# Performance work log

Hardware: AMD Instinct MI355X
Metric: run time of the kernel (lower is better)

Reference implementation:

```python
import jax, jax.numpy as jnp
import numpy as np

B, P, M, N, H = 2, 2048, 1024, 16, 64
NEG = 1e10


def setup_inputs() -> dict:
    key = jax.random.key(0)
    ks = jax.random.split(key, 8)
    std = 0.02
    return {
        "x": jax.random.normal(ks[0], (B, P, M), jnp.float32),
        "kernel_query": std * jax.random.normal(ks[1], (N, M, H), jnp.float32),
        "bias_query": jnp.zeros((N, H), jnp.float32),
        "kernel_key": std * jax.random.normal(ks[2], (N, M, H), jnp.float32),
        "bias_key": jnp.zeros((N, H), jnp.float32),
        "kernel_value": std * jax.random.normal(ks[3], (N, M, H), jnp.float32),
        "bias_value": jnp.zeros((N, H), jnp.float32),
        "kernel_out": std * jax.random.normal(ks[4], (N, H, M), jnp.float32),
        "bias_out": jnp.zeros((M,), jnp.float32),
    }


def reference(x, kernel_query, bias_query, kernel_key, bias_key,
              kernel_value, bias_value, kernel_out, bias_out):
    # per-head projections: [b,p,m] x [n,m,h] -> [b,p,n,h]
    q = jnp.einsum('bpm,nmh->bpnh', x, kernel_query) + bias_query
    k = jnp.einsum('bpm,nmh->bpnh', x, kernel_key) + bias_key
    v = jnp.einsum('bpm,nmh->bpnh', x, kernel_value) + bias_value

    # explicit score matrix [b,n,pq,pk]
    scores = jnp.einsum('bqnh,bknh->bnqk', q, k) / jnp.sqrt(jnp.float32(H))
    # faithful reproduction of original (inverted) mask: keep strictly-upper
    # triangle, subtract 1e10 elsewhere
    p = scores.shape[-1]
    mask = jnp.triu(jnp.ones((p, p), scores.dtype), k=1)  # [pq,pk]
    masked = scores * mask - NEG * (1.0 - mask)
    attn = jax.nn.softmax(masked, axis=-1)

    z = jnp.einsum('bknh,bnqk->bqnh', v, attn)
    return jnp.einsum('bqnh,nhm->bqm', z, kernel_out) + bias_out
```

## Files before the change

kernel.cpp:

```cpp
#include <hip/hip_runtime.h>

typedef __attribute__((ext_vector_type(8))) __bf16 bf16x8;
typedef __attribute__((ext_vector_type(4))) float  f32x4;
typedef unsigned short u16;
typedef unsigned int   u32;

__device__ __forceinline__ u16 f2b(float f) {
  u32 u = __builtin_bit_cast(u32, f);
  u32 r = (u + 0x7FFFu + ((u >> 16) & 1u)) >> 16;
  return (u16)r;
}

typedef __attribute__((address_space(3))) void lds_void;
typedef const __attribute__((address_space(1))) void gbl_void;

__device__ __forceinline__ void gload_lds16(const u16* g, u16* l) {
  __builtin_amdgcn_global_load_lds((gbl_void*)g, (lds_void*)l, 16, 0, 0);
}

#define QSCALE 0.18033688011112042f
#define MFIX   4.328085122666891f

__global__ __launch_bounds__(256) void prep_x(const float* __restrict__ x,
                                              u16* __restrict__ xb) {
  int i = blockIdx.x * 256 + threadIdx.x;
  float4 v = ((const float4*)x)[i];
  ushort4 o;
  o.x = f2b(v.x); o.y = f2b(v.y); o.z = f2b(v.z); o.w = f2b(v.w);
  ((ushort4*)xb)[i] = o;
}

__global__ __launch_bounds__(256) void tcast(const float* __restrict__ src,
                                             u16* __restrict__ dst,
                                             int R, int C, int sstride, int dstride,
                                             int smat, int dmat) {
  __shared__ float t[64][65];
  src += (size_t)blockIdx.y * smat;
  dst += (size_t)blockIdx.y * dmat;
  int ntr = R >> 6;
  int rt = blockIdx.x % ntr, ct = blockIdx.x / ntr;
  int r0 = rt * 64, c0 = ct * 64;
  int tid = threadIdx.x;
  int rr = tid >> 2, q = tid & 3;
#pragma unroll
  for (int i = 0; i < 4; ++i) {
    float4 v = *(const float4*)&src[(size_t)(r0 + rr) * sstride + c0 + q * 16 + i * 4];
    t[rr][q * 16 + i * 4 + 0] = v.x;
    t[rr][q * 16 + i * 4 + 1] = v.y;
    t[rr][q * 16 + i * 4 + 2] = v.z;
    t[rr][q * 16 + i * 4 + 3] = v.w;
  }
  __syncthreads();
  int cc = rr;
#pragma unroll
  for (int i = 0; i < 4; ++i) {
    ushort4 o;
    o.x = f2b(t[q * 16 + i * 4 + 0][cc]);
    o.y = f2b(t[q * 16 + i * 4 + 1][cc]);
    o.z = f2b(t[q * 16 + i * 4 + 2][cc]);
    o.w = f2b(t[q * 16 + i * 4 + 3][cc]);
    *(ushort4*)&dst[(size_t)(c0 + cc) * dstride + r0 + q * 16 + i * 4] = o;
  }
}

template <int KDIM>
__device__ __forceinline__ void gemm_main(const u16* __restrict__ A,
                                          const u16* __restrict__ Bm,
                                          int R0, int C0,
                                          u16* As, u16* Bs, f32x4 (&acc)[4][4]) {
  int tid = threadIdx.x;
  int w = tid >> 6, l = tid & 63;
  int lr = l & 15, lg = l >> 4;
  int wr = w >> 1, wc = w & 1;
  for (int k0 = 0; k0 < KDIM; k0 += 32) {
#pragma unroll
    for (int i = 0; i < 2; ++i) {
      int t = w * 2 + i;
      gload_lds16(A  + (size_t)(R0 + t * 16 + (l >> 2)) * KDIM + k0 + (l & 3) * 8, &As[t * 512]);
      gload_lds16(Bm + (size_t)(C0 + t * 16 + (l >> 2)) * KDIM + k0 + (l & 3) * 8, &Bs[t * 512]);
    }
    __syncthreads();
    bf16x8 af[4], bfr[4];
#pragma unroll
    for (int mi = 0; mi < 4; ++mi)
      af[mi] = *(const bf16x8*)&As[(wr * 64 + mi * 16 + lr) * 32 + lg * 8];
#pragma unroll
    for (int ni = 0; ni < 4; ++ni)
      bfr[ni] = *(const bf16x8*)&Bs[(wc * 64 + ni * 16 + lr) * 32 + lg * 8];
#pragma unroll
    for (int mi = 0; mi < 4; ++mi)
#pragma unroll
      for (int ni = 0; ni < 4; ++ni)
        acc[mi][ni] = __builtin_amdgcn_mfma_f32_16x16x32_bf16(af[mi], bfr[ni], acc[mi][ni], 0, 0, 0);
    __syncthreads();
  }
}

__global__ __launch_bounds__(256) void gemm_qkv(const u16* __restrict__ xb,
                                                const u16* __restrict__ wbt,
                                                const float* __restrict__ bq,
                                                const float* __restrict__ bk,
                                                const float* __restrict__ bv,
                                                u16* __restrict__ qb,
                                                u16* __restrict__ kbf,
                                                u16* __restrict__ vtb) {
  __shared__ __align__(16) u16 As[128 * 32];
  __shared__ __align__(16) u16 Bs[128 * 32];
  f32x4 acc[4][4];
#pragma unroll
  for (int mi = 0; mi < 4; ++mi)
#pragma unroll
    for (int ni = 0; ni < 4; ++ni) acc[mi][ni] = (f32x4){0.f, 0.f, 0.f, 0.f};

  int bid = blockIdx.x;
  int rt = bid & 31, ct = bid >> 5;
  int R0 = rt * 128, C0 = ct * 128;
  gemm_main<1024>(xb, wbt, R0, C0, As, Bs, acc);

  int tid = threadIdx.x;
  int w = tid >> 6, l = tid & 63;
  int lr = l & 15, lg = l >> 4;
  int wr = w >> 1, wc = w & 1;
#pragma unroll
  for (int ni = 0; ni < 4; ++ni) {
    int col = C0 + wc * 64 + ni * 16 + lr;
    int proj = col >> 10;
    int within = col & 1023;
    int n = within >> 6, h = within & 63;
    const float* bias = (proj == 0) ? bq : (proj == 1 ? bk : bv);
    float badd = bias[within];
    float scl = (proj == 0) ? QSCALE : 1.0f;
#pragma unroll
    for (int mi = 0; mi < 4; ++mi) {
#pragma unroll
      for (int r = 0; r < 4; ++r) {
        int row = R0 + wr * 64 + mi * 16 + lg * 4 + r;
        int b = row >> 11, p = row & 2047;
        int bn = b * 16 + n;
        u16 u = f2b((acc[mi][ni][r] + badd) * scl);
        if (proj == 0)      qb [((size_t)bn * 2048 + p) * 64 + h] = u;
        else if (proj == 1) kbf[((size_t)bn * 2048 + p) * 64 + h] = u;
        else                vtb[(((size_t)bn * 32 + (p >> 6)) * 64 + h) * 64 + (p & 63)] = u;
      }
    }
  }
}

__global__ __launch_bounds__(256) void mean_v(const u16* __restrict__ vtb,
                                              u16* __restrict__ zb) {
  __shared__ float red[4][64];
  int bn = blockIdx.x;
  int w = threadIdx.x >> 6, h = threadIdx.x & 63;
  const u16* base = vtb + (size_t)bn * 131072 + (size_t)h * 64;
  float acc = 0.f;
  for (int pb = w; pb < 32; pb += 4) {
    const u16* r = base + (size_t)pb * 4096;
#pragma unroll
    for (int c = 0; c < 8; ++c) {
      bf16x8 v = *(const bf16x8*)(r + c * 8);
#pragma unroll
      for (int j = 0; j < 8; ++j) acc += (float)v[j];
    }
  }
  red[w][h] = acc;
  __syncthreads();
  if (w == 0) {
    float s = (red[0][h] + red[1][h] + red[2][h] + red[3][h]) * (1.0f / 2048.0f);
    int b = bn >> 4, n = bn & 15;
    zb[((size_t)(b * 2048 + 2047) * 16 + n) * 64 + h] = f2b(s);
  }
}

#define ATTN_STEP(BUFC, MASKED)                                                \
  {                                                                            \
    if (t + 1 < trips) {                                                       \
      gload_lds16(sk,       &Ks[BUFC ^ 1][w * 1024]);                          \
      gload_lds16(sk + 512, &Ks[BUFC ^ 1][w * 1024 + 512]);                    \
      gload_lds16(sv,       &Vs[BUFC ^ 1][w * 1024]);                          \
      gload_lds16(sv + 512, &Vs[BUFC ^ 1][w * 1024 + 512]);                    \
      sk += 4096; sv += 4096;                                                  \
      asm volatile("s_waitcnt vmcnt(4)" ::: "memory");                         \
    } else {                                                                   \
      asm volatile("s_waitcnt vmcnt(0)" ::: "memory");                         \
    }                                                                          \
    __builtin_amdgcn_s_barrier();                                              \
    asm volatile("" ::: "memory");                                             \
    f32x4 sacc[4];                                                             \
    __builtin_amdgcn_s_setprio(1);                                             \
    _Pragma("unroll") for (int nb = 0; nb < 4; ++nb) {                         \
      int row = nb * 16 + lr, sw = row & 7;                                    \
      bf16x8 kf0 = *(const bf16x8*)&Ks[BUFC][row * 64 + ((lg ^ sw) << 3)];     \
      bf16x8 kf1 = *(const bf16x8*)&Ks[BUFC][row * 64 + (((lg + 4) ^ sw) << 3)]; \
      f32x4 s = (f32x4){0.f, 0.f, 0.f, 0.f};                                   \
      s = __builtin_amdgcn_mfma_f32_16x16x32_bf16(qf0, kf0, s, 0, 0, 0);       \
      s = __builtin_amdgcn_mfma_f32_16x16x32_bf16(qf1, kf1, s, 0, 0, 0);       \
      sacc[nb] = s;                                                            \
    }                                                                          \
    __builtin_amdgcn_s_setprio(0);                                             \
    u16 pbv[4][4];                                                             \
    if (MASKED) {                                                              \
      _Pragma("unroll") for (int nb = 0; nb < 4; ++nb) {                       \
        int key = nb * 16 + lr;                                                \
        _Pragma("unroll") for (int r = 0; r < 4; ++r) {                        \
          int qrow = w * 16 + lg * 4 + r;                                      \
          float xv = (key > qrow) ? sacc[nb][r] : -1.0e10f;                    \
          float pe = __builtin_amdgcn_exp2f(xv - MFIX);                        \
          rsum[r] += pe;                                                       \
          pbv[nb][r] = __builtin_bit_cast(u16, (__bf16)pe);                    \
        }                                                                      \
      }                                                                        \
    } else {                                                                   \
      _Pragma("unroll") for (int nb = 0; nb < 4; ++nb)                         \
        _Pragma("unroll") for (int r = 0; r < 4; ++r) {                        \
          float pe = __builtin_amdgcn_exp2f(sacc[nb][r] - MFIX);               \
          rsum[r] += pe;                                                       \
          pbv[nb][r] = __builtin_bit_cast(u16, (__bf16)pe);                    \
        }                                                                      \
    }                                                                          \
    _Pragma("unroll") for (int nb = 0; nb < 4; ++nb)                           \
      _Pragma("unroll") for (int r = 0; r < 4; ++r) {                          \
        int prow = lg * 4 + r;                                                 \
        Plds[w][prow * 64 + ((((nb * 2) + (lr >> 3)) ^ (prow & 7)) << 3) + (lr & 7)] = pbv[nb][r]; \
      }                                                                        \
    asm volatile("s_waitcnt lgkmcnt(0)" ::: "memory");                         \
    __builtin_amdgcn_sched_barrier(0);                                         \
    bf16x8 pf0 = *(const bf16x8*)&Plds[w][lr * 64 + ((lg ^ (lr & 7)) << 3)];   \
    bf16x8 pf1 = *(const bf16x8*)&Plds[w][lr * 64 + (((4 + lg) ^ (lr & 7)) << 3)]; \
    __builtin_amdgcn_s_setprio(1);                                             \
    _Pragma("unroll") for (int hb = 0; hb < 4; ++hb) {                         \
      int row = hb * 16 + lr, sw = row & 7;                                    \
      bf16x8 vf0 = *(const bf16x8*)&Vs[BUFC][row * 64 + ((lg ^ sw) << 3)];     \
      bf16x8 vf1 = *(const bf16x8*)&Vs[BUFC][row * 64 + (((lg + 4) ^ sw) << 3)]; \
      oacc[hb] = __builtin_amdgcn_mfma_f32_16x16x32_bf16(pf0, vf0, oacc[hb], 0, 0, 0); \
      oacc[hb] = __builtin_amdgcn_mfma_f32_16x16x32_bf16(pf1, vf1, oacc[hb], 0, 0, 0); \
    }                                                                          \
    __builtin_amdgcn_s_setprio(0);                                             \
    asm volatile("" ::: "memory");                                             \
    __builtin_amdgcn_s_barrier();                                              \
    ++t;                                                                       \
  }

__global__ __launch_bounds__(256, 4) void attn_kern(const u16* __restrict__ qb,
                                                    const u16* __restrict__ kbf,
                                                    const u16* __restrict__ vtb,
                                                    u16* __restrict__ zb) {
  __shared__ __align__(16) u16 Ks[2][4096];
  __shared__ __align__(16) u16 Vs[2][4096];
  __shared__ __align__(16) u16 Plds[4][1024];

  int bid = blockIdx.x;
  int bn = bid & 31, c = bid >> 5;
  int trips = 32 - c;
  int tid = threadIdx.x;
  int w = tid >> 6, l = tid & 63;
  int lr = l & 15, lg = l >> 4;

  const u16* Q  = qb  + (size_t)bn * 131072;
  const u16* Kp = kbf + (size_t)bn * 131072;
  const u16* Vt = vtb + (size_t)bn * 131072;

  int row0 = w * 16 + (l >> 3), col8 = l & 7;
  int soff = row0 * 64 + ((col8 ^ (row0 & 7)) << 3);

  int q0w = c * 64 + w * 16;
  bf16x8 qf0 = *(const bf16x8*)&Q[(size_t)(q0w + lr) * 64 + lg * 8];
  bf16x8 qf1 = *(const bf16x8*)&Q[(size_t)(q0w + lr) * 64 + 32 + lg * 8];

  float rsum[4];
  f32x4 oacc[4];
#pragma unroll
  for (int r = 0; r < 4; ++r) rsum[r] = 0.0f;
#pragma unroll
  for (int hb = 0; hb < 4; ++hb) oacc[hb] = (f32x4){0.f, 0.f, 0.f, 0.f};

  const u16* sk = Kp + (size_t)c * 4096 + soff;
  const u16* sv = Vt + (size_t)c * 4096 + soff;
  gload_lds16(sk,       &Ks[0][w * 1024]);
  gload_lds16(sk + 512, &Ks[0][w * 1024 + 512]);
  gload_lds16(sv,       &Vs[0][w * 1024]);
  gload_lds16(sv + 512, &Vs[0][w * 1024 + 512]);
  sk += 4096; sv += 4096;

  int t = 0;
  ATTN_STEP(0, true)
  while (t + 1 < trips) {
    ATTN_STEP(1, false)
    ATTN_STEP(0, false)
  }
  if (t < trips) ATTN_STEP(1, false)

#pragma unroll
  for (int r = 0; r < 4; ++r) {
    float v = rsum[r];
    v += __shfl_xor(v, 1);
    v += __shfl_xor(v, 2);
    v += __shfl_xor(v, 4);
    v += __shfl_xor(v, 8);
    rsum[r] = 1.0f / v;
  }
  int b = bn >> 4, n = bn & 15;
#pragma unroll
  for (int hb = 0; hb < 4; ++hb) {
    int h = hb * 16 + lr;
#pragma unroll
    for (int r = 0; r < 4; ++r) {
      int qrow = q0w + lg * 4 + r;
      zb[((size_t)(b * 2048 + qrow) * 16 + n) * 64 + h] = f2b(oacc[hb][r] * rsum[r]);
    }
  }
}

__global__ __launch_bounds__(256) void gemm_out(const u16* __restrict__ zb,
                                                const u16* __restrict__ wot,
                                                const float* __restrict__ bo,
                                                float* __restrict__ out) {
  __shared__ __align__(16) u16 As[128 * 32];
  __shared__ __align__(16) u16 Bs[128 * 32];
  f32x4 acc[4][4];
#pragma unroll
  for (int mi = 0; mi < 4; ++mi)
#pragma unroll
    for (int ni = 0; ni < 4; ++ni) acc[mi][ni] = (f32x4){0.f, 0.f, 0.f, 0.f};

  int bid = blockIdx.x;
  int rt = bid & 31, ct = bid >> 5;
  int R0 = rt * 128, C0 = ct * 128;
  gemm_main<1024>(zb, wot, R0, C0, As, Bs, acc);

  int tid = threadIdx.x;
  int w = tid >> 6, l = tid & 63;
  int lr = l & 15, lg = l >> 4;
  int wr = w >> 1, wc = w & 1;
#pragma unroll
  for (int ni = 0; ni < 4; ++ni) {
    int col = C0 + wc * 64 + ni * 16 + lr;
    float badd = bo[col];
#pragma unroll
    for (int mi = 0; mi < 4; ++mi) {
#pragma unroll
      for (int r = 0; r < 4; ++r) {
        int row = R0 + wr * 64 + mi * 16 + lg * 4 + r;
        out[(size_t)row * 1024 + col] = acc[mi][ni][r] + badd;
      }
    }
  }
}

extern "C" void kernel_launch(void* const* d_in, const int* in_sizes, int n_in,
                              void* d_out, int out_size, void* d_ws, size_t ws_size,
                              hipStream_t stream) {
  const float* x  = (const float*)d_in[0];
  const float* wq = (const float*)d_in[1];
  const float* bq = (const float*)d_in[2];
  const float* wk = (const float*)d_in[3];
  const float* bk = (const float*)d_in[4];
  const float* wv = (const float*)d_in[5];
  const float* bv = (const float*)d_in[6];
  const float* wo = (const float*)d_in[7];
  const float* bo = (const float*)d_in[8];
  float* out = (float*)d_out;

  char* ws = (char*)d_ws;
  u16* xb  = (u16*)(ws + ((size_t)0 << 20));
  u16* wbt = (u16*)(ws + ((size_t)8 << 20));
  u16* wot = (u16*)(ws + ((size_t)14 << 20));
  u16* qb  = (u16*)(ws + ((size_t)16 << 20));
  u16* kbf = (u16*)(ws + ((size_t)24 << 20));
  u16* vtb = (u16*)(ws + ((size_t)32 << 20));
  u16* zb  = (u16*)(ws + ((size_t)40 << 20));

  prep_x<<<dim3(4096), dim3(256), 0, stream>>>(x, xb);
  tcast<<<dim3(16, 16), dim3(256), 0, stream>>>(wq, wbt + (0u << 20), 1024, 64, 64, 1024, 65536, 65536);
  tcast<<<dim3(16, 16), dim3(256), 0, stream>>>(wk, wbt + (1u << 20), 1024, 64, 64, 1024, 65536, 65536);
  tcast<<<dim3(16, 16), dim3(256), 0, stream>>>(wv, wbt + (2u << 20), 1024, 64, 64, 1024, 65536, 65536);
  tcast<<<dim3(256, 1), dim3(256), 0, stream>>>(wo, wot, 1024, 1024, 1024, 1024, 0, 0);

  gemm_qkv<<<dim3(32 * 24), dim3(256), 0, stream>>>(xb, wbt, bq, bk, bv, qb, kbf, vtb);
  attn_kern<<<dim3(1024), dim3(256), 0, stream>>>(qb, kbf, vtb, zb);
  mean_v<<<dim3(32), dim3(256), 0, stream>>>(vtb, zb);
  gemm_out<<<dim3(32 * 8), dim3(256), 0, stream>>>(zb, wot, bo, out);
}
```

Before: 128.0 us.

## Double-buffer GEMM LDS loads and stage QKV epilogue through LDS for vector stores

The shared GEMM mainloop now uses two LDS stages, prefetching the next K-slice with global_load_lds while MFMAs run on the current one, using explicit vmcnt waits and raw barriers. The QKV epilogue writes each wave's 64x64 tile into LDS, transposed for V, then emits coalesced 16-byte global stores instead of scattered 2-byte stores. This doubles LDS per block, which may reduce occupancy. The epilogue assumes each 64-column wave tile lies within a single head and projection.

New measurement: 132.0 us. 3.2% more time.

```diff
diff --git a/kernel.cpp b/kernel.cpp
--- a/kernel.cpp
+++ b/kernel.cpp
@@ -67,32 +67,47 @@
 __device__ __forceinline__ void gemm_main(const u16* __restrict__ A,
                                           const u16* __restrict__ Bm,
                                           int R0, int C0,
-                                          u16* As, u16* Bs, f32x4 (&acc)[4][4]) {
+                                          u16 (*Stage)[8192], f32x4 (&acc)[4][4]) {
+  const int NS = KDIM / 32;
   int tid = threadIdx.x;
   int w = tid >> 6, l = tid & 63;
   int lr = l & 15, lg = l >> 4;
   int wr = w >> 1, wc = w & 1;
-  for (int k0 = 0; k0 < KDIM; k0 += 32) {
+
+  auto stage = [&](int step, int bsel) {
 #pragma unroll
     for (int i = 0; i < 2; ++i) {
       int t = w * 2 + i;
-      gload_lds16(A  + (size_t)(R0 + t * 16 + (l >> 2)) * KDIM + k0 + (l & 3) * 8, &As[t * 512]);
-      gload_lds16(Bm + (size_t)(C0 + t * 16 + (l >> 2)) * KDIM + k0 + (l & 3) * 8, &Bs[t * 512]);
-    }
-    __syncthreads();
+      gload_lds16(A  + (size_t)(R0 + t * 16 + (l >> 2)) * KDIM + step * 32 + (l & 3) * 8, &Stage[bsel][t * 512]);
+      gload_lds16(Bm + (size_t)(C0 + t * 16 + (l >> 2)) * KDIM + step * 32 + (l & 3) * 8, &Stage[bsel][4096 + t * 512]);
+    }
+  };
+
+  stage(0, 0);
+  for (int t = 0; t < NS; ++t) {
+    int buf = t & 1;
+    if (t + 1 < NS) {
+      stage(t + 1, buf ^ 1);
+      asm volatile("s_waitcnt vmcnt(4)" ::: "memory");
+    } else {
+      asm volatile("s_waitcnt vmcnt(0)" ::: "memory");
+    }
+    __builtin_amdgcn_s_barrier();
+    asm volatile("" ::: "memory");
     bf16x8 af[4], bfr[4];
 #pragma unroll
     for (int mi = 0; mi < 4; ++mi)
-      af[mi] = *(const bf16x8*)&As[(wr * 64 + mi * 16 + lr) * 32 + lg * 8];
+      af[mi] = *(const bf16x8*)&Stage[buf][(wr * 64 + mi * 16 + lr) * 32 + lg * 8];
 #pragma unroll
     for (int ni = 0; ni < 4; ++ni)
-      bfr[ni] = *(const bf16x8*)&Bs[(wc * 64 + ni * 16 + lr) * 32 + lg * 8];
+      bfr[ni] = *(const bf16x8*)&Stage[buf][4096 + (wc * 64 + ni * 16 + lr) * 32 + lg * 8];
 #pragma unroll
     for (int mi = 0; mi < 4; ++mi)
 #pragma unroll
       for (int ni = 0; ni < 4; ++ni)
         acc[mi][ni] = __builtin_amdgcn_mfma_f32_16x16x32_bf16(af[mi], bfr[ni], acc[mi][ni], 0, 0, 0);
-    __syncthreads();
+    asm volatile("" ::: "memory");
+    __builtin_amdgcn_s_barrier();
   }
 }
 
@@ -104,8 +119,7 @@
                                                 u16* __restrict__ qb,
                                                 u16* __restrict__ kbf,
                                                 u16* __restrict__ vtb) {
-  __shared__ __align__(16) u16 As[128 * 32];
-  __shared__ __align__(16) u16 Bs[128 * 32];
+  __shared__ __align__(16) u16 Stage[2][8192];
   f32x4 acc[4][4];
 #pragma unroll
   for (int mi = 0; mi < 4; ++mi)
@@ -115,33 +129,62 @@
   int bid = blockIdx.x;
   int rt = bid & 31, ct = bid >> 5;
   int R0 = rt * 128, C0 = ct * 128;
-  gemm_main<1024>(xb, wbt, R0, C0, As, Bs, acc);
+  gemm_main<1024>(xb, wbt, R0, C0, Stage, acc);
 
   int tid = threadIdx.x;
   int w = tid >> 6, l = tid & 63;
   int lr = l & 15, lg = l >> 4;
   int wr = w >> 1, wc = w & 1;
-#pragma unroll
-  for (int ni = 0; ni < 4; ++ni) {
-    int col = C0 + wc * 64 + ni * 16 + lr;
-    int proj = col >> 10;
-    int within = col & 1023;
-    int n = within >> 6, h = within & 63;
-    const float* bias = (proj == 0) ? bq : (proj == 1 ? bk : bv);
-    float badd = bias[within];
-    float scl = (proj == 0) ? QSCALE : 1.0f;
-#pragma unroll
-    for (int mi = 0; mi < 4; ++mi) {
-#pragma unroll
-      for (int r = 0; r < 4; ++r) {
-        int row = R0 + wr * 64 + mi * 16 + lg * 4 + r;
-        int b = row >> 11, p = row & 2047;
-        int bn = b * 16 + n;
-        u16 u = f2b((acc[mi][ni][r] + badd) * scl);
-        if (proj == 0)      qb [((size_t)bn * 2048 + p) * 64 + h] = u;
-        else if (proj == 1) kbf[((size_t)bn * 2048 + p) * 64 + h] = u;
-        else                vtb[(((size_t)bn * 32 + (p >> 6)) * 64 + h) * 64 + (p & 63)] = u;
-      }
+
+  u16* Tw = &Stage[0][0] + w * 4096;
+
+  int proj = C0 >> 10;
+  int colbase = C0 + wc * 64;
+  int n = (colbase & 1023) >> 6;
+  int rowbase = R0 + wr * 64;
+  int b = rowbase >> 11, p0 = rowbase & 2047;
+  int bn = b * 16 + n;
+  const float* bias = (proj == 0) ? bq : (proj == 1 ? bk : bv);
+  float scl = (proj == 0) ? QSCALE : 1.0f;
+
+  if (proj < 2) {
+#pragma unroll
+    for (int ni = 0; ni < 4; ++ni) {
+      float badd = bias[n * 64 + ni * 16 + lr];
+#pragma unroll
+      for (int mi = 0; mi < 4; ++mi)
+#pragma unroll
+        for (int r = 0; r < 4; ++r)
+          Tw[(mi * 16 + lg * 4 + r) * 64 + ni * 16 + lr] = f2b((acc[mi][ni][r] + badd) * scl);
+    }
+    asm volatile("s_waitcnt lgkmcnt(0)" ::: "memory");
+    __builtin_amdgcn_sched_barrier(0);
+    u16* dst = ((proj == 0) ? qb : kbf) + ((size_t)bn * 2048 + p0) * 64;
+#pragma unroll
+    for (int pp = 0; pp < 8; ++pp) {
+      int ri = pp * 8 + (l >> 3);
+      *(bf16x8*)&dst[(size_t)ri * 64 + (l & 7) * 8] =
+          *(const bf16x8*)&Tw[ri * 64 + (l & 7) * 8];
+    }
+  } else {
+#pragma unroll
+    for (int ni = 0; ni < 4; ++ni) {
+      float badd = bias[n * 64 + ni * 16 + lr];
+#pragma unroll
+      for (int mi = 0; mi < 4; ++mi)
+#pragma unroll
+        for (int r = 0; r < 4; ++r)
+          Tw[(ni * 16 + lr) * 64 + mi * 16 + lg * 4 + r] = f2b(acc[mi][ni][r] + badd);
+    }
+    asm volatile("s_waitcnt lgkmcnt(0)" ::: "memory");
+    __builtin_amdgcn_sched_barrier(0);
+    int pblk = p0 >> 6;
+    u16* dst = vtb + ((size_t)bn * 32 + pblk) * 4096;
+#pragma unroll
+    for (int pp = 0; pp < 8; ++pp) {
+      int ci = pp * 8 + (l >> 3);
+      *(bf16x8*)&dst[(size_t)ci * 64 + (l & 7) * 8] =
+          *(const bf16x8*)&Tw[ci * 64 + (l & 7) * 8];
     }
   }
 }
@@ -314,8 +357,7 @@
                                                 const u16* __restrict__ wot,
                                                 const float* __restrict__ bo,
                                                 float* __restrict__ out) {
-  __shared__ __align__(16) u16 As[128 * 32];
-  __shared__ __align__(16) u16 Bs[128 * 32];
+  __shared__ __align__(16) u16 Stage[2][8192];
   f32x4 acc[4][4];
 #pragma unroll
   for (int mi = 0; mi < 4; ++mi)
@@ -325,7 +367,7 @@
   int bid = blockIdx.x;
   int rt = bid & 31, ct = bid >> 5;
   int R0 = rt * 128, C0 = ct * 128;
-  gemm_main<1024>(zb, wot, R0, C0, As, Bs, acc);
+  gemm_main<1024>(zb, wot, R0, C0, Stage, acc);
 
   int tid = threadIdx.x;
   int w = tid >> 6, l = tid & 63;
```

## Merge prep kernels into one launch and stage V-transpose epilogue through LDS

Applied to the files above, without the earlier changes.

Folds the x cast and the four weight transpose-cast kernels into a single prep_all launch, using block index ranges to pick the work. This removes four kernel launches and the gaps between them. It also rewrites the QKV GEMM epilogue with per-block-uniform projection and index math. For V, values are transposed through swizzled shared memory so that global stores become 16-byte row writes instead of scattered 2-byte writes. The cost is extra LDS traffic and a wait in the epilogue, plus one heavier prep kernel with divergent block roles.

Measured after the change: 128.3 us. Within noise of the previous version (+0.3%).

```diff
diff --git a/kernel.cpp b/kernel.cpp
--- a/kernel.cpp
+++ b/kernel.cpp
@@ -21,26 +21,39 @@
 #define QSCALE 0.18033688011112042f
 #define MFIX   4.328085122666891f
 
-__global__ __launch_bounds__(256) void prep_x(const float* __restrict__ x,
-                                              u16* __restrict__ xb) {
-  int i = blockIdx.x * 256 + threadIdx.x;
-  float4 v = ((const float4*)x)[i];
-  ushort4 o;
-  o.x = f2b(v.x); o.y = f2b(v.y); o.z = f2b(v.z); o.w = f2b(v.w);
-  ((ushort4*)xb)[i] = o;
-}
-
-__global__ __launch_bounds__(256) void tcast(const float* __restrict__ src,
-                                             u16* __restrict__ dst,
-                                             int R, int C, int sstride, int dstride,
-                                             int smat, int dmat) {
+__global__ __launch_bounds__(256) void prep_all(const float* __restrict__ x,
+                                                const float* __restrict__ wq,
+                                                const float* __restrict__ wk,
+                                                const float* __restrict__ wv,
+                                                const float* __restrict__ wo,
+                                                u16* __restrict__ xb,
+                                                u16* __restrict__ wbt,
+                                                u16* __restrict__ wot) {
+  int bid = blockIdx.x;
+  int tid = threadIdx.x;
+  if (bid < 4096) {
+    int i = bid * 256 + tid;
+    float4 v = ((const float4*)x)[i];
+    ushort4 o;
+    o.x = f2b(v.x); o.y = f2b(v.y); o.z = f2b(v.z); o.w = f2b(v.w);
+    ((ushort4*)xb)[i] = o;
+    return;
+  }
   __shared__ float t[64][65];
-  src += (size_t)blockIdx.y * smat;
-  dst += (size_t)blockIdx.y * dmat;
-  int ntr = R >> 6;
-  int rt = blockIdx.x % ntr, ct = blockIdx.x / ntr;
-  int r0 = rt * 64, c0 = ct * 64;
-  int tid = threadIdx.x;
+  int sub = bid - 4096;
+  const float* src; u16* dst; int sstride, dstride, r0, c0;
+  if (sub < 768) {
+    int proj = sub >> 8, rem = sub & 255;
+    int ym = rem >> 4, xt = rem & 15;
+    src = ((proj == 0) ? wq : (proj == 1) ? wk : wv) + (size_t)ym * 65536;
+    dst = wbt + ((size_t)proj << 20) + (size_t)ym * 65536;
+    sstride = 64; dstride = 1024; r0 = xt * 64; c0 = 0;
+  } else {
+    int s2 = sub - 768;
+    src = wo; dst = wot;
+    sstride = 1024; dstride = 1024;
+    r0 = (s2 & 15) * 64; c0 = (s2 >> 4) * 64;
+  }
   int rr = tid >> 2, q = tid & 3;
 #pragma unroll
   for (int i = 0; i < 4; ++i) {
@@ -104,8 +117,7 @@
                                                 u16* __restrict__ qb,
                                                 u16* __restrict__ kbf,
                                                 u16* __restrict__ vtb) {
-  __shared__ __align__(16) u16 As[128 * 32];
-  __shared__ __align__(16) u16 Bs[128 * 32];
+  __shared__ __align__(16) u16 SH[2][4096];
   f32x4 acc[4][4];
 #pragma unroll
   for (int mi = 0; mi < 4; ++mi)
@@ -115,32 +127,62 @@
   int bid = blockIdx.x;
   int rt = bid & 31, ct = bid >> 5;
   int R0 = rt * 128, C0 = ct * 128;
-  gemm_main<1024>(xb, wbt, R0, C0, As, Bs, acc);
+  gemm_main<1024>(xb, wbt, R0, C0, SH[0], SH[1], acc);
 
   int tid = threadIdx.x;
   int w = tid >> 6, l = tid & 63;
   int lr = l & 15, lg = l >> 4;
   int wr = w >> 1, wc = w & 1;
-#pragma unroll
-  for (int ni = 0; ni < 4; ++ni) {
-    int col = C0 + wc * 64 + ni * 16 + lr;
-    int proj = col >> 10;
-    int within = col & 1023;
-    int n = within >> 6, h = within & 63;
-    const float* bias = (proj == 0) ? bq : (proj == 1 ? bk : bv);
-    float badd = bias[within];
+
+  int proj = C0 >> 10;
+  int colbase = C0 + wc * 64;
+  int n = (colbase & 1023) >> 6;
+  int rowbase = R0 + wr * 64;
+  int b = rowbase >> 11, p0 = rowbase & 2047;
+  int bn = b * 16 + n;
+
+  if (proj < 2) {
+    const float* bias = (proj == 0) ? bq : bk;
     float scl = (proj == 0) ? QSCALE : 1.0f;
-#pragma unroll
-    for (int mi = 0; mi < 4; ++mi) {
-#pragma unroll
-      for (int r = 0; r < 4; ++r) {
-        int row = R0 + wr * 64 + mi * 16 + lg * 4 + r;
-        int b = row >> 11, p = row & 2047;
-        int bn = b * 16 + n;
-        u16 u = f2b((acc[mi][ni][r] + badd) * scl);
-        if (proj == 0)      qb [((size_t)bn * 2048 + p) * 64 + h] = u;
-        else if (proj == 1) kbf[((size_t)bn * 2048 + p) * 64 + h] = u;
-        else                vtb[(((size_t)bn * 32 + (p >> 6)) * 64 + h) * 64 + (p & 63)] = u;
+    u16* dst = ((proj == 0) ? qb : kbf) + ((size_t)bn * 2048 + p0) * 64;
+#pragma unroll
+    for (int ni = 0; ni < 4; ++ni) {
+      float badd = bias[n * 64 + ni * 16 + lr];
+#pragma unroll
+      for (int mi = 0; mi < 4; ++mi)
+#pragma unroll
+        for (int r = 0; r < 4; ++r)
+          dst[(size_t)(mi * 16 + lg * 4 + r) * 64 + ni * 16 + lr] =
+              f2b((acc[mi][ni][r] + badd) * scl);
+    }
+  } else {
+    int pblk = p0 >> 6;
+    u16* dst = vtb + ((size_t)bn * 32 + pblk) * 4096;
+    u16* Tw = &SH[0][0] + w * 2048;
+#pragma unroll
+    for (int hh = 0; hh < 2; ++hh) {
+#pragma unroll
+      for (int nn = 0; nn < 2; ++nn) {
+        int ni = hh * 2 + nn;
+        float badd = bv[n * 64 + ni * 16 + lr];
+        int hloc = nn * 16 + lr;
+#pragma unroll
+        for (int mi = 0; mi < 4; ++mi)
+#pragma unroll
+          for (int r = 0; r < 4; ++r) {
+            int ploc = mi * 16 + lg * 4 + r;
+            Tw[hloc * 64 + ((((ploc >> 3) ^ (hloc & 7)) << 3) | (ploc & 7))] =
+                f2b(acc[mi][ni][r] + badd);
+          }
+      }
+      asm volatile("s_waitcnt lgkmcnt(0)" ::: "memory");
+      __builtin_amdgcn_sched_barrier(0);
+#pragma unroll
+      for (int pp = 0; pp < 4; ++pp) {
+        int hloc = pp * 8 + (l >> 3);
+        int ccn = l & 7;
+        bf16x8 vv = *(const bf16x8*)&Tw[hloc * 64 + ((ccn ^ (hloc & 7)) << 3)];
+        *(bf16x8*)&dst[(size_t)(hh * 32 + hloc) * 64 + ccn * 8] = vv;
       }
     }
   }
@@ -369,12 +411,7 @@
   u16* vtb = (u16*)(ws + ((size_t)32 << 20));
   u16* zb  = (u16*)(ws + ((size_t)40 << 20));
 
-  prep_x<<<dim3(4096), dim3(256), 0, stream>>>(x, xb);
-  tcast<<<dim3(16, 16), dim3(256), 0, stream>>>(wq, wbt + (0u << 20), 1024, 64, 64, 1024, 65536, 65536);
-  tcast<<<dim3(16, 16), dim3(256), 0, stream>>>(wk, wbt + (1u << 20), 1024, 64, 64, 1024, 65536, 65536);
-  tcast<<<dim3(16, 16), dim3(256), 0, stream>>>(wv, wbt + (2u << 20), 1024, 64, 64, 1024, 65536, 65536);
-  tcast<<<dim3(256, 1), dim3(256), 0, stream>>>(wo, wot, 1024, 1024, 1024, 1024, 0, 0);
-
+  prep_all<<<dim3(5120), dim3(256), 0, stream>>>(x, wq, wk, wv, wo, xb, wbt, wot);
   gemm_qkv<<<dim3(32 * 24), dim3(256), 0, stream>>>(xb, wbt, bq, bk, bv, qb, kbf, vtb);
   attn_kern<<<dim3(1024), dim3(256), 0, stream>>>(qb, kbf, vtb, zb);
   mean_v<<<dim3(32), dim3(256), 0, stream>>>(vtb, zb);
```
